# Kernel tuning notes

Measured on AMD Instinct MI355X. Metric: run time of the kernel, lower is better.

The kernel has to match this reference:

```python
import jax, jax.numpy as jnp
import numpy as np

C = 256; G = 8; K = 3; P = K * K; GC = C // G
PAD = K // 2; PAD_DW = 1
EPS_LN = 1e-5; EPS_DWLN = 1e-6; EPS_BN = 1e-5
OFFSET_SCALE = 1.0


def _ln(x, g, b, eps=EPS_LN):
    mu = x.mean(-1, keepdims=True)
    var = ((x - mu) ** 2).mean(-1, keepdims=True)
    return (x - mu) * jax.lax.rsqrt(var + eps) * g + b


def _bn(x, g, b, m, v):  # x: NCHW, eval-mode batchnorm with running stats
    s = jax.lax.rsqrt(v + EPS_BN)
    return (x - m[None, :, None, None]) * (g * s)[None, :, None, None] + b[None, :, None, None]


def _dcnv3_core(x, offset, mask):
    # x: (N,H,W,C) projected input; offset: (N,H,W,G*P*2); mask: (N,H,W,G,P) softmaxed
    N, H, W, _ = x.shape
    Hp, Wp = H + 2 * PAD, W + 2 * PAD
    x_pad = jnp.pad(x, ((0, 0), (PAD, PAD), (PAD, PAD), (0, 0)))
    img = x_pad.reshape(N, Hp, Wp, G, GC).transpose(0, 3, 4, 1, 2)  # (N,G,gc,Hp,Wp)
    # reference points, normalized by padded spatial dims (stride=1, dilation=1)
    start = (K - 1) // 2 + 0.5
    ref_x = (start + jnp.arange(W, dtype=x.dtype)) / Wp
    ref_y = (start + jnp.arange(H, dtype=x.dtype)) / Hp
    rx, ry = jnp.meshgrid(ref_x, ref_y, indexing='xy')  # (H,W)
    ref = jnp.stack([rx, ry], -1)  # (H,W,2) as (x,y)
    # dilation grid (kernel tap offsets), tap index p = i_w*K + j_h per torch meshgrid order
    gw = (jnp.arange(K, dtype=x.dtype) - (K - 1) // 2) / Wp
    gh = (jnp.arange(K, dtype=x.dtype) - (K - 1) // 2) / Hp
    gxx, gyy = jnp.meshgrid(gw, gh, indexing='ij')
    grid = jnp.stack([gxx, gyy], -1).reshape(P, 2)
    norm = jnp.array([Wp, Hp], dtype=x.dtype)
    off = offset.reshape(N, H, W, G, P, 2) * (OFFSET_SCALE / norm)
    loc = ref[None, :, :, None, None, :] + grid * OFFSET_SCALE + off  # (N,H,W,G,P,2)
    sg = (2.0 * loc - 1.0).transpose(0, 3, 1, 2, 4, 5).reshape(N, G, H * W, P, 2)

    def sample_one(im, gr):  # im: (gc,Hp,Wp), gr: (HW,P,2) in [-1,1]
        gx = (gr[..., 0] + 1.0) * (Wp / 2) - 0.5  # align_corners=False
        gy = (gr[..., 1] + 1.0) * (Hp / 2) - 0.5
        x0 = jnp.floor(gx); y0 = jnp.floor(gy)
        wx = gx - x0; wy = gy - y0
        def gat(ix, iy):
            valid = ((ix >= 0) & (ix <= Wp - 1) & (iy >= 0) & (iy <= Hp - 1)).astype(im.dtype)
            ixc = jnp.clip(ix, 0, Wp - 1).astype(jnp.int32)
            iyc = jnp.clip(iy, 0, Hp - 1).astype(jnp.int32)
            return im[:, iyc, ixc] * valid  # (gc,HW,P), zero padding outside
        return (gat(x0, y0) * ((1 - wx) * (1 - wy))
                + gat(x0 + 1, y0) * (wx * (1 - wy))
                + gat(x0, y0 + 1) * ((1 - wx) * wy)
                + gat(x0 + 1, y0 + 1) * (wx * wy))

    sampled = jax.vmap(jax.vmap(sample_one))(img, sg)  # (N,G,gc,HW,P)
    m = mask.transpose(0, 3, 1, 2, 4).reshape(N, G, 1, H * W, P)
    out = (sampled * m).sum(-1)  # (N,G,gc,HW)
    return out.transpose(0, 3, 1, 2).reshape(N, H, W, C)


def _dcnv3(inp, dw_w, dw_b, dwln_g, dwln_b, off_w, off_b, msk_w, msk_b, inp_w, inp_b, outp_w, outp_b):
    N, H, W, _ = inp.shape
    x = inp @ inp_w + inp_b  # input_proj
    # depthwise conv offset/mask branch (on the raw input, not the projection)
    x1 = jax.lax.conv_general_dilated(inp, dw_w, (1, 1), ((PAD_DW, PAD_DW), (PAD_DW, PAD_DW)),
                                      dimension_numbers=('NHWC', 'HWIO', 'NHWC'),
                                      feature_group_count=C) + dw_b
    x1 = jax.nn.gelu(_ln(x1, dwln_g, dwln_b, EPS_DWLN), approximate=False)
    offset = x1 @ off_w + off_b  # (N,H,W,G*P*2)
    mask = jax.nn.softmax((x1 @ msk_w + msk_b).reshape(N, H, W, G, P), axis=-1)
    return _dcnv3_core(x, offset, mask) @ outp_w + outp_b  # output_proj


def _forward(x, conv1_w, bn1_g, bn1_b, bn1_m, bn1_v, ln1_g, ln1_b, dw_w, dw_b, dwln_g, dwln_b,
             off_w, off_b, msk_w, msk_b, inp_w, inp_b, outp_w, outp_b, gamma1,
             ln2_g, ln2_b, fc1_w, fc1_b, fc2_w, fc2_b, gamma2, bn2_g, bn2_b, bn2_m, bn2_v):
    out = jax.lax.conv_general_dilated(x, conv1_w, (1, 1), ((1, 1), (1, 1)),
                                       dimension_numbers=('NCHW', 'OIHW', 'NCHW'))
    out = jax.nn.relu(_bn(out, bn1_g, bn1_b, bn1_m, bn1_v))
    t = out.transpose(0, 2, 3, 1)  # NHWC for the InternImage layer
    # post_norm InternImage layer with layer_scale
    d = _dcnv3(t, dw_w, dw_b, dwln_g, dwln_b, off_w, off_b, msk_w, msk_b, inp_w, inp_b, outp_w, outp_b)
    t = t + gamma1 * _ln(d, ln1_g, ln1_b)
    h = jax.nn.gelu(t @ fc1_w + fc1_b, approximate=False) @ fc2_w + fc2_b
    t = t + gamma2 * _ln(h, ln2_g, ln2_b)
    out = _bn(t.transpose(0, 3, 1, 2), bn2_g, bn2_b, bn2_m, bn2_v)
    return jax.nn.relu(out + x)  # residual (downsample is None: stride=1, inplanes==planes)


def setup_inputs() -> dict:
    key = jax.random.key(0)
    ks = iter(jax.random.split(key, 48))
    rn = lambda shape, s=1.0: jax.random.normal(next(ks), shape, dtype=jnp.float32) * s
    hid = 4 * C
    d = {}
    d['x'] = rn((8, C, 56, 56))
    d['conv1_w'] = rn((C, C, 3, 3), (2.0 / (9 * C)) ** 0.5)
    d['bn1_g'] = jnp.ones((C,), jnp.float32); d['bn1_b'] = jnp.zeros((C,), jnp.float32)
    d['bn1_m'] = rn((C,), 0.1)
    d['bn1_v'] = jax.random.uniform(next(ks), (C,), jnp.float32, 0.5, 1.5)
    d['ln1_g'] = jnp.ones((C,), jnp.float32); d['ln1_b'] = jnp.zeros((C,), jnp.float32)
    d['dw_w'] = rn((3, 3, 1, C), (1.0 / 9) ** 0.5); d['dw_b'] = jnp.zeros((C,), jnp.float32)
    d['dwln_g'] = jnp.ones((C,), jnp.float32); d['dwln_b'] = jnp.zeros((C,), jnp.float32)
    d['off_w'] = rn((C, G * P * 2), 0.01); d['off_b'] = rn((G * P * 2,), 0.01)
    d['msk_w'] = rn((C, G * P), 0.01); d['msk_b'] = jnp.zeros((G * P,), jnp.float32)
    d['inp_w'] = rn((C, C), C ** -0.5); d['inp_b'] = jnp.zeros((C,), jnp.float32)
    d['outp_w'] = rn((C, C), C ** -0.5); d['outp_b'] = jnp.zeros((C,), jnp.float32)
    d['gamma1'] = rn((C,), 0.01)
    d['ln2_g'] = jnp.ones((C,), jnp.float32); d['ln2_b'] = jnp.zeros((C,), jnp.float32)
    d['fc1_w'] = rn((C, hid), C ** -0.5); d['fc1_b'] = jnp.zeros((hid,), jnp.float32)
    d['fc2_w'] = rn((hid, C), hid ** -0.5); d['fc2_b'] = jnp.zeros((C,), jnp.float32)
    d['gamma2'] = rn((C,), 0.01)
    d['bn2_g'] = jnp.ones((C,), jnp.float32); d['bn2_b'] = jnp.zeros((C,), jnp.float32)
    d['bn2_m'] = rn((C,), 0.1)
    d['bn2_v'] = jax.random.uniform(next(ks), (C,), jnp.float32, 0.5, 1.5)
    return d


def reference(x, conv1_w, bn1_g, bn1_b, bn1_m, bn1_v, ln1_g, ln1_b, dw_w, dw_b, dwln_g, dwln_b,
              off_w, off_b, msk_w, msk_b, inp_w, inp_b, outp_w, outp_b, gamma1,
              ln2_g, ln2_b, fc1_w, fc1_b, fc2_w, fc2_b, gamma2, bn2_g, bn2_b, bn2_m, bn2_v):
    return _forward(x, conv1_w, bn1_g, bn1_b, bn1_m, bn1_v, ln1_g, ln1_b, dw_w, dw_b, dwln_g, dwln_b,
                    off_w, off_b, msk_w, msk_b, inp_w, inp_b, outp_w, outp_b, gamma1,
                    ln2_g, ln2_b, fc1_w, fc1_b, fc2_w, fc2_b, gamma2, bn2_g, bn2_b, bn2_m, bn2_v)
```

## Files before the change

### kernel.cpp

```cpp
#include <hip/hip_runtime.h>
#include <cmath>

#define N_   8
#define H_   56
#define W_   56
#define C_   256
#define HW_  3136
#define NHW_ 25088
#define G_   8
#define GC_  32
#define P_   9
#define HID_ 1024
#define XP_H 58
#define XP_W 58

typedef __attribute__((ext_vector_type(8))) short bf16x8;
typedef __attribute__((ext_vector_type(4))) float f32x4;

#define GLOAD_LDS16(g, l) __builtin_amdgcn_global_load_lds( \
    (const __attribute__((address_space(1))) void*)(g), \
    (__attribute__((address_space(3))) void*)(l), 16, 0, 0)

__device__ __forceinline__ unsigned short f2bf(float f) {
    unsigned u = __float_as_uint(f);
    u += 0x7FFF + ((u >> 16) & 1);
    return (unsigned short)(u >> 16);
}

__device__ __forceinline__ float gelu_exact(float v) {
    return 0.5f * v * (1.f + erff(v * 0.70710678118654752f));
}

__device__ __forceinline__ float2 block_sum2(float a, float b, float* sm) {
    int lane = threadIdx.x & 63;
    int wid  = threadIdx.x >> 6;
#pragma unroll
    for (int off = 32; off > 0; off >>= 1) {
        a += __shfl_down(a, off, 64);
        b += __shfl_down(b, off, 64);
    }
    if (lane == 0) { sm[wid] = a; sm[wid + 4] = b; }
    __syncthreads();
    float ra = sm[0] + sm[1] + sm[2] + sm[3];
    float rb = sm[4] + sm[5] + sm[6] + sm[7];
    __syncthreads();
    return make_float2(ra, rb);
}

__global__ __launch_bounds__(256) void k_prep_xpad(const float* __restrict__ x, unsigned short* __restrict__ xpad) {
    int nh = blockIdx.x;
    int n = nh / H_, h = nh - n * H_;
    int c = threadIdx.x;
    const float* xr = x + ((size_t)(n * C_ + c)) * HW_ + h * W_;
    unsigned short* orow = xpad + ((size_t)((n * XP_H + h + 1) * XP_W + 1)) * C_ + c;
    for (int w = 0; w < W_; ++w) orow[(size_t)w * C_] = f2bf(xr[w]);
}

__global__ __launch_bounds__(256) void k_prep_wTT(const float* __restrict__ w, unsigned short* __restrict__ wTT) {
    int i  = blockIdx.x * 256 + threadIdx.x;
    int ci = i & 255;
    int r  = i >> 8;
    int co = r & 255;
    int kk = r >> 8;
    wTT[i] = f2bf(w[(co * 256 + ci) * 9 + kk]);
}

__global__ __launch_bounds__(256) void k_prep_sqT(const float* __restrict__ src, unsigned short* __restrict__ dst) {
    int n = blockIdx.x, k = threadIdx.x;
    dst[n * C_ + k] = f2bf(src[k * C_ + n]);
}

__global__ __launch_bounds__(256) void k_prep_fc1T(const float* __restrict__ src, unsigned short* __restrict__ dst) {
    int n = blockIdx.x, k = threadIdx.x;
    dst[(size_t)n * C_ + k] = f2bf(src[(size_t)k * HID_ + n]);
}

__global__ __launch_bounds__(256) void k_prep_fc2T(const float* __restrict__ src, unsigned short* __restrict__ dst) {
    int n = blockIdx.x, k0 = threadIdx.x;
#pragma unroll
    for (int q = 0; q < 4; ++q) {
        int k = q * 256 + k0;
        dst[(size_t)n * HID_ + k] = f2bf(src[(size_t)k * C_ + n]);
    }
}

__global__ __launch_bounds__(256) void k_prep_om(const float* __restrict__ offw, const float* __restrict__ offb,
                                                 const float* __restrict__ mskw, const float* __restrict__ mskb,
                                                 unsigned short* __restrict__ omT, float* __restrict__ omb) {
    int n = blockIdx.x, k = threadIdx.x;
    float v = 0.f;
    if (n < 144)      v = offw[k * 144 + n];
    else if (n < 216) v = mskw[k * 72 + (n - 144)];
    omT[n * C_ + k] = f2bf(v);
    if (k == 0) omb[n] = (n < 144) ? offb[n] : (n < 216 ? mskb[n - 144] : 0.f);
}

__global__ __launch_bounds__(256) void k_conv1_mfma(const unsigned short* __restrict__ xpad,
                                                    const unsigned short* __restrict__ wTT,
                                                    const float* __restrict__ g, const float* __restrict__ b,
                                                    const float* __restrict__ m, const float* __restrict__ v,
                                                    float* __restrict__ t, unsigned short* __restrict__ t_bf) {
    __shared__ __align__(16) unsigned char smem[24576];
    unsigned short* sm16 = (unsigned short*)smem;
    bf16x8* sA = (bf16x8*)smem;
    bf16x8* sB = (bf16x8*)(smem + 8192);
    int tid = threadIdx.x;
    int wave = tid >> 6, lane = tid & 63;
    int r = lane & 15, kq = lane >> 4;
    int mt = blockIdx.x >> 1, nt = blockIdx.x & 1;
    int m0 = mt * 64, n0 = nt * 128;
    int wm = wave & 1, wn = wave >> 1;

    int pix = m0 + wave * 16 + r;
    int n = pix / HW_, hw = pix - n * HW_;
    int h = hw / W_, w = hw - h * W_;
    size_t abase = ((size_t)((n * XP_H + h) * XP_W + w)) * C_;

    f32x4 acc[2][4] = {};
#pragma unroll 1
    for (int kt = 0; kt < 36; ++kt) {
        int tap = kt >> 2, ktk = kt & 3;
        int kh = tap / 3, kw = tap - kh * 3;
        int k0 = ktk * 64;
        const unsigned short* ap = xpad + abase + (size_t)(kh * XP_W + kw) * C_ + k0;
        if (kt) __syncthreads();
#pragma unroll
        for (int i = 0; i < 2; ++i) {
            int q = wave * 2 + i;
            GLOAD_LDS16(ap + (i * 4 + kq) * 8, sm16 + q * 512);
        }
#pragma unroll
        for (int i = 0; i < 4; ++i) {
            int q = wave * 4 + i;
            int nrow = n0 + (q >> 1) * 16 + r;
            int cc   = (q & 1) * 4 + kq;
            GLOAD_LDS16(wTT + ((size_t)(tap * C_) + nrow) * C_ + k0 + cc * 8, sm16 + 4096 + q * 512);
        }
        __syncthreads();
#pragma unroll
        for (int ks = 0; ks < 2; ++ks) {
            bf16x8 af[2], bfr[4];
#pragma unroll
            for (int mi = 0; mi < 2; ++mi) af[mi]  = sA[((wm * 2 + mi) * 2 + ks) * 64 + lane];
#pragma unroll
            for (int ni = 0; ni < 4; ++ni) bfr[ni] = sB[((wn * 4 + ni) * 2 + ks) * 64 + lane];
#pragma unroll
            for (int mi = 0; mi < 2; ++mi)
#pragma unroll
                for (int ni = 0; ni < 4; ++ni)
                    acc[mi][ni] = __builtin_amdgcn_mfma_f32_16x16x32_bf16(af[mi], bfr[ni], acc[mi][ni], 0, 0, 0);
        }
    }

#pragma unroll
    for (int ni = 0; ni < 4; ++ni) {
        int co = n0 + (wn * 4 + ni) * 16 + r;
        float sc = g[co] * rsqrtf(v[co] + 1e-5f);
        float sh = b[co] - m[co] * sc;
#pragma unroll
        for (int mi = 0; mi < 2; ++mi) {
#pragma unroll
            for (int reg = 0; reg < 4; ++reg) {
                int po = m0 + (wm * 2 + mi) * 16 + kq * 4 + reg;
                float val = fmaxf(acc[mi][ni][reg] * sc + sh, 0.f);
                size_t idx = (size_t)po * C_ + co;
                t[idx] = val;
                t_bf[idx] = f2bf(val);
            }
        }
    }
}

__global__ __launch_bounds__(256) void k_inproj_mfma(const unsigned short* __restrict__ t_bf,
                                                     const unsigned short* __restrict__ inpwT,
                                                     const float* __restrict__ bias,
                                                     float* __restrict__ xproj) {
    int wave = threadIdx.x >> 6, lane = threadIdx.x & 63;
    int r = lane & 15, kq = lane >> 4;
    int p0 = blockIdx.x * 32, co0 = wave * 64;
    f32x4 acc[2][4] = {};
#pragma unroll 1
    for (int ks = 0; ks < 8; ++ks) {
        bf16x8 a0 = *(const bf16x8*)(t_bf + (size_t)(p0 + r) * C_ + ks * 32 + kq * 8);
        bf16x8 a1 = *(const bf16x8*)(t_bf + (size_t)(p0 + 16 + r) * C_ + ks * 32 + kq * 8);
        const unsigned short* bp = inpwT + (size_t)(co0 + r) * C_ + ks * 32 + kq * 8;
#pragma unroll
        for (int ni = 0; ni < 4; ++ni) {
            bf16x8 b = *(const bf16x8*)(bp + (size_t)ni * 16 * C_);
            acc[0][ni] = __builtin_amdgcn_mfma_f32_16x16x32_bf16(a0, b, acc[0][ni], 0, 0, 0);
            acc[1][ni] = __builtin_amdgcn_mfma_f32_16x16x32_bf16(a1, b, acc[1][ni], 0, 0, 0);
        }
    }
#pragma unroll
    for (int ni = 0; ni < 4; ++ni) {
        int col = co0 + ni * 16 + r;
        float bb = bias[col];
#pragma unroll
        for (int mi = 0; mi < 2; ++mi)
#pragma unroll
            for (int reg = 0; reg < 4; ++reg) {
                int pix = p0 + mi * 16 + kq * 4 + reg;
                xproj[(size_t)pix * C_ + col] = acc[mi][ni][reg] + bb;
            }
    }
}

__global__ __launch_bounds__(256) void k_dw(const float* __restrict__ t, const float* __restrict__ dww,
                                            const float* __restrict__ dwb, const float* __restrict__ lg,
                                            const float* __restrict__ lb, unsigned short* __restrict__ x1_bf) {
    __shared__ float sm[8];
    int pix = blockIdx.x;
    int n = pix / HW_, hw = pix - n * HW_;
    int h = hw / W_,  w = hw - h * W_;
    int c = threadIdx.x;
    float acc = dwb[c];
#pragma unroll
    for (int kh = 0; kh < 3; ++kh) {
        int y = h + kh - 1;
        if ((unsigned)y >= H_) continue;
#pragma unroll
        for (int kw = 0; kw < 3; ++kw) {
            int xx = w + kw - 1;
            if ((unsigned)xx >= W_) continue;
            acc = fmaf(t[(size_t)(n * HW_ + y * W_ + xx) * C_ + c], dww[(kh * 3 + kw) * C_ + c], acc);
        }
    }
    float2 r  = block_sum2(acc, acc * acc, sm);
    float mu  = r.x * (1.f / C_);
    float var = fmaxf(r.y * (1.f / C_) - mu * mu, 0.f);
    float rs  = rsqrtf(var + 1e-6f);
    float val = (acc - mu) * rs * lg[c] + lb[c];
    x1_bf[(size_t)pix * C_ + c] = f2bf(gelu_exact(val));
}

__global__ __launch_bounds__(256) void k_offmask_mfma(const unsigned short* __restrict__ x1_bf,
                                                      const unsigned short* __restrict__ omT,
                                                      const float* __restrict__ omb,
                                                      float* __restrict__ offo, float* __restrict__ msko) {
    __shared__ float som[32][225];
    int wave = threadIdx.x >> 6, lane = threadIdx.x & 63;
    int r = lane & 15, kq = lane >> 4;
    int p0 = blockIdx.x * 32, co0 = wave * 64;
    f32x4 acc[2][4] = {};
#pragma unroll 1
    for (int ks = 0; ks < 8; ++ks) {
        bf16x8 a0 = *(const bf16x8*)(x1_bf + (size_t)(p0 + r) * C_ + ks * 32 + kq * 8);
        bf16x8 a1 = *(const bf16x8*)(x1_bf + (size_t)(p0 + 16 + r) * C_ + ks * 32 + kq * 8);
        const unsigned short* bp = omT + (size_t)(co0 + r) * C_ + ks * 32 + kq * 8;
#pragma unroll
        for (int ni = 0; ni < 4; ++ni) {
            bf16x8 b = *(const bf16x8*)(bp + (size_t)ni * 16 * C_);
            acc[0][ni] = __builtin_amdgcn_mfma_f32_16x16x32_bf16(a0, b, acc[0][ni], 0, 0, 0);
            acc[1][ni] = __builtin_amdgcn_mfma_f32_16x16x32_bf16(a1, b, acc[1][ni], 0, 0, 0);
        }
    }
#pragma unroll
    for (int ni = 0; ni < 4; ++ni) {
        int col = co0 + ni * 16 + r;
        if (col < 216) {
            float bb = omb[col];
#pragma unroll
            for (int mi = 0; mi < 2; ++mi)
#pragma unroll
                for (int reg = 0; reg < 4; ++reg)
                    som[mi * 16 + kq * 4 + reg][col] = acc[mi][ni][reg] + bb;
        }
    }
    __syncthreads();
    int tid = threadIdx.x;
#pragma unroll
    for (int i = 0; i < 18; ++i) {
        int j = i * 256 + tid;
        int px = j / 144, col = j - px * 144;
        offo[(size_t)(p0 + px) * 144 + col] = som[px][col];
    }
    int px = tid >> 3, g = tid & 7;
    float mx = -1e30f;
#pragma unroll
    for (int p = 0; p < 9; ++p) mx = fmaxf(mx, som[px][144 + g * 9 + p]);
    float e[9], s = 0.f;
#pragma unroll
    for (int p = 0; p < 9; ++p) { e[p] = expf(som[px][144 + g * 9 + p] - mx); s += e[p]; }
    float inv = 1.f / s;
#pragma unroll
    for (int p = 0; p < 9; ++p) msko[(size_t)(p0 + px) * 72 + g * 9 + p] = e[p] * inv;
}

__global__ __launch_bounds__(256) void k_core(const float* __restrict__ xp,
                                              const float* __restrict__ offo, const float* __restrict__ msko,
                                              unsigned short* __restrict__ core_bf) {
    int pix = blockIdx.x;
    int n = pix / HW_, hw = pix - n * HW_;
    int h = hw / W_,  w = hw - h * W_;
    int g  = threadIdx.x >> 5;
    int cc = threadIdx.x & 31;
    const float* op = offo + (size_t)pix * 144 + g * 18;
    const float* mp = msko + (size_t)pix * 72 + g * 9;
    const float* xg = xp + (size_t)n * HW_ * C_ + g * GC_ + cc;
    float acc = 0.f;
#pragma unroll
    for (int p = 0; p < 9; ++p) {
        float gx = (float)(w + (p / 3)) + op[p * 2];
        float gy = (float)(h + (p % 3)) + op[p * 2 + 1];
        float fx = floorf(gx), fy = floorf(gy);
        float wx = gx - fx,   wy = gy - fy;
        int ix = (int)fx - 1, iy = (int)fy - 1;
        float v00 = 0.f, v10 = 0.f, v01 = 0.f, v11 = 0.f;
        bool x0ok = (unsigned)ix < W_, x1ok = (unsigned)(ix + 1) < W_;
        bool y0ok = (unsigned)iy < H_, y1ok = (unsigned)(iy + 1) < H_;
        if (y0ok) {
            const float* rr = xg + (size_t)(iy * W_) * C_;
            if (x0ok) v00 = rr[(size_t)ix * C_];
            if (x1ok) v10 = rr[(size_t)(ix + 1) * C_];
        }
        if (y1ok) {
            const float* rr = xg + (size_t)((iy + 1) * W_) * C_;
            if (x0ok) v01 = rr[(size_t)ix * C_];
            if (x1ok) v11 = rr[(size_t)(ix + 1) * C_];
        }
        float sval = (v00 * (1.f - wx) + v10 * wx) * (1.f - wy)
                   + (v01 * (1.f - wx) + v11 * wx) * wy;
        acc = fmaf(mp[p], sval, acc);
    }
    core_bf[(size_t)pix * C_ + threadIdx.x] = f2bf(acc);
}

__global__ __launch_bounds__(256) void k_outproj_mfma(const unsigned short* __restrict__ core_bf,
                                                      const unsigned short* __restrict__ outpwT,
                                                      const float* __restrict__ bo,
                                                      const float* __restrict__ g1, const float* __restrict__ lg,
                                                      const float* __restrict__ lb,
                                                      float* __restrict__ t, unsigned short* __restrict__ t_bf) {
    __shared__ float sd[32][260];
    int wave = threadIdx.x >> 6, lane = threadIdx.x & 63;
    int r = lane & 15, kq = lane >> 4;
    int p0 = blockIdx.x * 32, co0 = wave * 64;
    f32x4 acc[2][4] = {};
#pragma unroll 1
    for (int ks = 0; ks < 8; ++ks) {
        bf16x8 a0 = *(const bf16x8*)(core_bf + (size_t)(p0 + r) * C_ + ks * 32 + kq * 8);
        bf16x8 a1 = *(const bf16x8*)(core_bf + (size_t)(p0 + 16 + r) * C_ + ks * 32 + kq * 8);
        const unsigned short* bp = outpwT + (size_t)(co0 + r) * C_ + ks * 32 + kq * 8;
#pragma unroll
        for (int ni = 0; ni < 4; ++ni) {
            bf16x8 b = *(const bf16x8*)(bp + (size_t)ni * 16 * C_);
            acc[0][ni] = __builtin_amdgcn_mfma_f32_16x16x32_bf16(a0, b, acc[0][ni], 0, 0, 0);
            acc[1][ni] = __builtin_amdgcn_mfma_f32_16x16x32_bf16(a1, b, acc[1][ni], 0, 0, 0);
        }
    }
#pragma unroll
    for (int ni = 0; ni < 4; ++ni) {
        int col = co0 + ni * 16 + r;
        float bb = bo[col];
#pragma unroll
        for (int mi = 0; mi < 2; ++mi)
#pragma unroll
            for (int reg = 0; reg < 4; ++reg)
                sd[mi * 16 + kq * 4 + reg][col] = acc[mi][ni][reg] + bb;
    }
    __syncthreads();
    int px = threadIdx.x >> 3, sub = threadIdx.x & 7;
    float s1 = 0.f, s2 = 0.f;
#pragma unroll
    for (int i = 0; i < 8; ++i) {
        float4 vv = *(const float4*)&sd[px][sub * 32 + i * 4];
        s1 += vv.x + vv.y + vv.z + vv.w;
        s2 += vv.x * vv.x + vv.y * vv.y + vv.z * vv.z + vv.w * vv.w;
    }
#pragma unroll
    for (int off = 1; off < 8; off <<= 1) { s1 += __shfl_xor(s1, off, 64); s2 += __shfl_xor(s2, off, 64); }
    float mu  = s1 * (1.f / C_);
    float var = fmaxf(s2 * (1.f / C_) - mu * mu, 0.f);
    float rs  = rsqrtf(var + 1e-5f);
#pragma unroll
    for (int i = 0; i < 32; ++i) {
        int col = sub * 32 + i;
        size_t idx = (size_t)(p0 + px) * C_ + col;
        float tn = t[idx] + g1[col] * ((sd[px][col] - mu) * rs * lg[col] + lb[col]);
        t[idx] = tn;
        t_bf[idx] = f2bf(tn);
    }
}

__global__ __launch_bounds__(256) void k_fc1_mfma(const unsigned short* __restrict__ t_bf,
                                                  const unsigned short* __restrict__ fc1wT,
                                                  const float* __restrict__ fc1b,
                                                  unsigned short* __restrict__ h_bf) {
    __shared__ __align__(16) unsigned char smem[34816];
    unsigned short* sm16 = (unsigned short*)smem;
    bf16x8* sA = (bf16x8*)smem;
    bf16x8* sB = (bf16x8*)(smem + 16384);
    int tid = threadIdx.x;
    int wave = tid >> 6, lane = tid & 63;
    int r = lane & 15, kq = lane >> 4;
    int mt = blockIdx.x >> 3, nt = blockIdx.x & 7;
    int m0 = mt * 128, n0 = nt * 128;
    int wm = wave & 1, wn = wave >> 1;

    f32x4 acc[4][4] = {};
#pragma unroll 1
    for (int kt = 0; kt < 4; ++kt) {
        int k0 = kt * 64;
        if (kt) __syncthreads();
#pragma unroll
        for (int i = 0; i < 4; ++i) {
            int q = wave * 4 + i;
            int row = m0 + (q >> 1) * 16 + r;
            int cc  = (q & 1) * 4 + kq;
            GLOAD_LDS16(t_bf + (size_t)row * C_ + k0 + cc * 8, sm16 + q * 512);
        }
#pragma unroll
        for (int i = 0; i < 4; ++i) {
            int q = wave * 4 + i;
            int nrow = n0 + (q >> 1) * 16 + r;
            int cc   = (q & 1) * 4 + kq;
            GLOAD_LDS16(fc1wT + (size_t)nrow * C_ + k0 + cc * 8, sm16 + 8192 + q * 512);
        }
        __syncthreads();
#pragma unroll
        for (int ks = 0; ks < 2; ++ks) {
            bf16x8 af[4], bfr[4];
#pragma unroll
            for (int mi = 0; mi < 4; ++mi) af[mi]  = sA[((wm * 4 + mi) * 2 + ks) * 64 + lane];
#pragma unroll
            for (int ni = 0; ni < 4; ++ni) bfr[ni] = sB[((wn * 4 + ni) * 2 + ks) * 64 + lane];
#pragma unroll
            for (int mi = 0; mi < 4; ++mi)
#pragma unroll
                for (int ni = 0; ni < 4; ++ni)
                    acc[mi][ni] = __builtin_amdgcn_mfma_f32_16x16x32_bf16(af[mi], bfr[ni], acc[mi][ni], 0, 0, 0);
        }
    }
    __syncthreads();
#pragma unroll
    for (int ni = 0; ni < 4; ++ni) {
        int col = (wn * 4 + ni) * 16 + r;
        float bb = fc1b[n0 + col];
#pragma unroll
        for (int mi = 0; mi < 4; ++mi)
#pragma unroll
            for (int reg = 0; reg < 4; ++reg) {
                int row = (wm * 4 + mi) * 16 + kq * 4 + reg;
                sm16[row * 136 + col] = f2bf(gelu_exact(acc[mi][ni][reg] + bb));
            }
    }
    __syncthreads();
    int trow = tid >> 1, thalf = tid & 1;
    const unsigned short* src = sm16 + trow * 136 + thalf * 64;
    unsigned short* dst = h_bf + (size_t)(m0 + trow) * HID_ + n0 + thalf * 64;
#pragma unroll
    for (int j = 0; j < 8; ++j)
        *(bf16x8*)(dst + j * 8) = *(const bf16x8*)(src + j * 8);
}

__global__ __launch_bounds__(256) void k_fc2ln_mfma(const unsigned short* __restrict__ h_bf,
                                                    const unsigned short* __restrict__ fc2wT,
                                                    const float* __restrict__ fc2b,
                                                    const float* __restrict__ g2, const float* __restrict__ lg,
                                                    const float* __restrict__ lb, float* __restrict__ t) {
    __shared__ __align__(16) unsigned char smem[40960];
    unsigned short* sm16 = (unsigned short*)smem;
    bf16x8* sA = (bf16x8*)smem;
    bf16x8* sB = (bf16x8*)(smem + 8192);
    int tid = threadIdx.x;
    int wave = tid >> 6, lane = tid & 63;
    int r = lane & 15, kq = lane >> 4;
    int m0 = blockIdx.x * 64;

    f32x4 acc[16] = {};
#pragma unroll 1
    for (int kt = 0; kt < 16; ++kt) {
        int k0 = kt * 64;
        if (kt) __syncthreads();
#pragma unroll
        for (int i = 0; i < 2; ++i) {
            int q = wave * 2 + i;
            int row = m0 + (q >> 1) * 16 + r;
            int cc  = (q & 1) * 4 + kq;
            GLOAD_LDS16(h_bf + (size_t)row * HID_ + k0 + cc * 8, sm16 + q * 512);
        }
#pragma unroll
        for (int i = 0; i < 8; ++i) {
            int q = wave * 8 + i;
            int nrow = (q >> 1) * 16 + r;
            int cc   = (q & 1) * 4 + kq;
            GLOAD_LDS16(fc2wT + (size_t)nrow * HID_ + k0 + cc * 8, sm16 + 4096 + q * 512);
        }
        __syncthreads();
#pragma unroll
        for (int ks = 0; ks < 2; ++ks) {
            bf16x8 a = sA[(wave * 2 + ks) * 64 + lane];
#pragma unroll
            for (int ni = 0; ni < 16; ++ni) {
                bf16x8 b = sB[(ni * 2 + ks) * 64 + lane];
                acc[ni] = __builtin_amdgcn_mfma_f32_16x16x32_bf16(a, b, acc[ni], 0, 0, 0);
            }
        }
    }
    float bb[16], g2v[16], lgv[16], lbv[16];
#pragma unroll
    for (int ni = 0; ni < 16; ++ni) {
        int col = ni * 16 + r;
        bb[ni] = fc2b[col]; g2v[ni] = g2[col]; lgv[ni] = lg[col]; lbv[ni] = lb[col];
    }
#pragma unroll
    for (int ni = 0; ni < 16; ++ni)
#pragma unroll
        for (int reg = 0; reg < 4; ++reg) acc[ni][reg] += bb[ni];
#pragma unroll
    for (int reg = 0; reg < 4; ++reg) {
        float s1 = 0.f, s2 = 0.f;
#pragma unroll
        for (int ni = 0; ni < 16; ++ni) { float vv = acc[ni][reg]; s1 += vv; s2 += vv * vv; }
#pragma unroll
        for (int off = 1; off < 16; off <<= 1) { s1 += __shfl_xor(s1, off, 64); s2 += __shfl_xor(s2, off, 64); }
        float mu  = s1 * (1.f / C_);
        float var = fmaxf(s2 * (1.f / C_) - mu * mu, 0.f);
        float rs  = rsqrtf(var + 1e-5f);
        int row = m0 + wave * 16 + kq * 4 + reg;
        float* tr = t + (size_t)row * C_;
#pragma unroll
        for (int ni = 0; ni < 16; ++ni) {
            int col = ni * 16 + r;
            tr[col] += g2v[ni] * ((acc[ni][reg] - mu) * rs * lgv[ni] + lbv[ni]);
        }
    }
}

__global__ __launch_bounds__(256) void k_final(const float* __restrict__ t, const float* __restrict__ x,
                                               const float* __restrict__ g, const float* __restrict__ b,
                                               const float* __restrict__ m, const float* __restrict__ v,
                                               float* __restrict__ out) {
    int i  = blockIdx.x * 256 + threadIdx.x;
    int hw = i % HW_;
    int r  = i / HW_;
    int c  = r & 255;
    int n  = r >> 8;
    float tv  = t[(size_t)(n * HW_ + hw) * C_ + c];
    float s   = rsqrtf(v[c] + 1e-5f);
    float val = (tv - m[c]) * (g[c] * s) + b[c] + x[i];
    out[i] = fmaxf(val, 0.f);
}

extern "C" void kernel_launch(void* const* d_in, const int* in_sizes, int n_in,
                              void* d_out, int out_size, void* d_ws, size_t ws_size,
                              hipStream_t stream) {
    const float* x      = (const float*)d_in[0];
    const float* conv1w = (const float*)d_in[1];
    const float* bn1g   = (const float*)d_in[2];
    const float* bn1b   = (const float*)d_in[3];
    const float* bn1m   = (const float*)d_in[4];
    const float* bn1v   = (const float*)d_in[5];
    const float* ln1g   = (const float*)d_in[6];
    const float* ln1b   = (const float*)d_in[7];
    const float* dww    = (const float*)d_in[8];
    const float* dwb    = (const float*)d_in[9];
    const float* dwlng  = (const float*)d_in[10];
    const float* dwlnb  = (const float*)d_in[11];
    const float* offw   = (const float*)d_in[12];
    const float* offb   = (const float*)d_in[13];
    const float* mskw   = (const float*)d_in[14];
    const float* mskb   = (const float*)d_in[15];
    const float* inpw   = (const float*)d_in[16];
    const float* inpb   = (const float*)d_in[17];
    const float* outpw  = (const float*)d_in[18];
    const float* outpb  = (const float*)d_in[19];
    const float* gamma1 = (const float*)d_in[20];
    const float* ln2g   = (const float*)d_in[21];
    const float* ln2b   = (const float*)d_in[22];
    const float* fc1w   = (const float*)d_in[23];
    const float* fc1b   = (const float*)d_in[24];
    const float* fc2w   = (const float*)d_in[25];
    const float* fc2b   = (const float*)d_in[26];
    const float* gamma2 = (const float*)d_in[27];
    const float* bn2g   = (const float*)d_in[28];
    const float* bn2b   = (const float*)d_in[29];
    const float* bn2m   = (const float*)d_in[30];
    const float* bn2v   = (const float*)d_in[31];
    float* out = (float*)d_out;

    float* ws    = (float*)d_ws;
    float* xproj = ws;
    float* offo  = xproj + (size_t)NHW_ * C_;
    float* msko  = offo  + (size_t)NHW_ * 144;
    unsigned short* x1_bf = (unsigned short*)(msko + (size_t)NHW_ * 72);
    unsigned short* scr   = x1_bf + (size_t)NHW_ * C_;
    float* t     = (float*)(scr + (size_t)N_ * XP_H * XP_W * C_);
    float* omb   = t + (size_t)NHW_ * C_;
    unsigned short* t_bf  = (unsigned short*)(omb + 256);
    unsigned short* wTT   = t_bf  + (size_t)NHW_ * C_;
    unsigned short* inpwT = wTT   + (size_t)9 * C_ * C_;
    unsigned short* outpwT= inpwT + (size_t)C_ * C_;
    unsigned short* fc1wT = outpwT+ (size_t)C_ * C_;
    unsigned short* fc2wT = fc1wT + (size_t)HID_ * C_;
    unsigned short* omT   = fc2wT + (size_t)C_ * HID_;
    unsigned short* xpad    = scr;
    unsigned short* core_bf = scr;
    unsigned short* h_bf    = (unsigned short*)xproj;

    hipMemsetAsync(xpad, 0, (size_t)N_ * XP_H * XP_W * C_ * sizeof(unsigned short), stream);
    k_prep_xpad<<<N_ * H_, 256, 0, stream>>>(x, xpad);
    k_prep_wTT <<<2304,    256, 0, stream>>>(conv1w, wTT);
    k_prep_sqT <<<256,     256, 0, stream>>>(inpw, inpwT);
    k_prep_sqT <<<256,     256, 0, stream>>>(outpw, outpwT);
    k_prep_fc1T<<<1024,    256, 0, stream>>>(fc1w, fc1wT);
    k_prep_fc2T<<<256,     256, 0, stream>>>(fc2w, fc2wT);
    k_prep_om  <<<256,     256, 0, stream>>>(offw, offb, mskw, mskb, omT, omb);

    k_conv1_mfma  <<<(NHW_ / 64) * 2, 256, 0, stream>>>(xpad, wTT, bn1g, bn1b, bn1m, bn1v, t, t_bf);
    k_inproj_mfma <<<NHW_ / 32, 256, 0, stream>>>(t_bf, inpwT, inpb, xproj);
    k_dw          <<<NHW_,      256, 0, stream>>>(t, dww, dwb, dwlng, dwlnb, x1_bf);
    k_offmask_mfma<<<NHW_ / 32, 256, 0, stream>>>(x1_bf, omT, omb, offo, msko);
    k_core        <<<NHW_,      256, 0, stream>>>(xproj, offo, msko, core_bf);
    k_outproj_mfma<<<NHW_ / 32, 256, 0, stream>>>(core_bf, outpwT, outpb, gamma1, ln1g, ln1b, t, t_bf);
    k_fc1_mfma    <<<(NHW_ / 128) * 8, 256, 0, stream>>>(t_bf, fc1wT, fc1b, h_bf);
    k_fc2ln_mfma  <<<NHW_ / 64, 256, 0, stream>>>(h_bf, fc2wT, fc2b, gamma2, ln2g, ln2b, t);
    k_final       <<<NHW_,      256, 0, stream>>>(t, x, bn2g, bn2b, bn2m, bn2v, out);
}
```

Measured before the change: 657.8 us.

## Double-buffer LDS staging in conv1 and fc2 GEMMs; restructure inproj to LDS

Conv1 and fc2+LN GEMMs now prefetch the next K-tile into a second LDS buffer using async global-to-LDS loads with explicit vmcnt waits, so loads overlap with MFMA work. The in-projection kernel is rewritten from direct global fragment loads into a 64-row-tile, LDS-staged, double-buffered GEMM like fc2. This hides global load latency at the cost of larger LDS allocations, up to 80KB per block, which may reduce occupancy. The inproj grid shrinks to 64-pixel tiles.

Measured after the change: 647.0 us. About the same (-1.6%).

```diff
diff --git a/kernel.cpp b/kernel.cpp
--- a/kernel.cpp
+++ b/kernel.cpp
@@ -100,10 +100,8 @@
                                                     const float* __restrict__ g, const float* __restrict__ b,
                                                     const float* __restrict__ m, const float* __restrict__ v,
                                                     float* __restrict__ t, unsigned short* __restrict__ t_bf) {
-    __shared__ __align__(16) unsigned char smem[24576];
+    __shared__ __align__(16) unsigned char smem[49152];
     unsigned short* sm16 = (unsigned short*)smem;
-    bf16x8* sA = (bf16x8*)smem;
-    bf16x8* sB = (bf16x8*)(smem + 8192);
     int tid = threadIdx.x;
     int wave = tid >> 6, lane = tid & 63;
     int r = lane & 15, kq = lane >> 4;
@@ -117,26 +115,39 @@
     size_t abase = ((size_t)((n * XP_H + h) * XP_W + w)) * C_;
 
     f32x4 acc[2][4] = {};
-#pragma unroll 1
-    for (int kt = 0; kt < 36; ++kt) {
+
+    auto stage = [&](int kt, int buf) {
         int tap = kt >> 2, ktk = kt & 3;
         int kh = tap / 3, kw = tap - kh * 3;
         int k0 = ktk * 64;
+        unsigned short* dstA = sm16 + buf * 12288;
+        unsigned short* dstB = dstA + 4096;
         const unsigned short* ap = xpad + abase + (size_t)(kh * XP_W + kw) * C_ + k0;
-        if (kt) __syncthreads();
-#pragma unroll
-        for (int i = 0; i < 2; ++i) {
-            int q = wave * 2 + i;
-            GLOAD_LDS16(ap + (i * 4 + kq) * 8, sm16 + q * 512);
-        }
+#pragma unroll
+        for (int i = 0; i < 2; ++i)
+            GLOAD_LDS16(ap + (i * 4 + kq) * 8, dstA + (wave * 2 + i) * 512);
 #pragma unroll
         for (int i = 0; i < 4; ++i) {
             int q = wave * 4 + i;
             int nrow = n0 + (q >> 1) * 16 + r;
             int cc   = (q & 1) * 4 + kq;
-            GLOAD_LDS16(wTT + ((size_t)(tap * C_) + nrow) * C_ + k0 + cc * 8, sm16 + 4096 + q * 512);
-        }
-        __syncthreads();
+            GLOAD_LDS16(wTT + ((size_t)(tap * C_) + nrow) * C_ + k0 + cc * 8, dstB + q * 512);
+        }
+    };
+
+    stage(0, 0);
+    int cur = 0;
+#pragma unroll 1
+    for (int kt = 0; kt < 36; ++kt) {
+        if (kt < 35) {
+            stage(kt + 1, cur ^ 1);
+            asm volatile("s_waitcnt vmcnt(6)" ::: "memory");
+        } else {
+            asm volatile("s_waitcnt vmcnt(0)" ::: "memory");
+        }
+        __builtin_amdgcn_s_barrier();
+        bf16x8* sA = (bf16x8*)(sm16 + cur * 12288);
+        bf16x8* sB = sA + 512;
 #pragma unroll
         for (int ks = 0; ks < 2; ++ks) {
             bf16x8 af[2], bfr[4];
@@ -150,6 +161,8 @@
                 for (int ni = 0; ni < 4; ++ni)
                     acc[mi][ni] = __builtin_amdgcn_mfma_f32_16x16x32_bf16(af[mi], bfr[ni], acc[mi][ni], 0, 0, 0);
         }
+        __builtin_amdgcn_s_barrier();
+        cur ^= 1;
     }
 
 #pragma unroll
@@ -175,33 +188,69 @@
                                                      const unsigned short* __restrict__ inpwT,
                                                      const float* __restrict__ bias,
                                                      float* __restrict__ xproj) {
-    int wave = threadIdx.x >> 6, lane = threadIdx.x & 63;
+    __shared__ __align__(16) unsigned char smem[81920];
+    unsigned short* sm16 = (unsigned short*)smem;
+    int tid = threadIdx.x;
+    int wave = tid >> 6, lane = tid & 63;
     int r = lane & 15, kq = lane >> 4;
-    int p0 = blockIdx.x * 32, co0 = wave * 64;
-    f32x4 acc[2][4] = {};
+    int m0 = blockIdx.x * 64;
+
+    f32x4 acc[16] = {};
+
+    auto stage = [&](int kt, int buf) {
+        int k0 = kt * 64;
+        unsigned short* dstA = sm16 + buf * 20480;
+        unsigned short* dstB = dstA + 4096;
+#pragma unroll
+        for (int i = 0; i < 2; ++i) {
+            int q = wave * 2 + i;
+            int row = m0 + wave * 16 + r;
+            GLOAD_LDS16(t_bf + (size_t)row * C_ + k0 + (i * 4 + kq) * 8, dstA + q * 512);
+        }
+#pragma unroll
+        for (int i = 0; i < 8; ++i) {
+            int q = wave * 8 + i;
+            int nrow = (q >> 1) * 16 + r;
+            int cc   = (q & 1) * 4 + kq;
+            GLOAD_LDS16(inpwT + (size_t)nrow * C_ + k0 + cc * 8, dstB + q * 512);
+        }
+    };
+
+    stage(0, 0);
+    int cur = 0;
 #pragma unroll 1
-    for (int ks = 0; ks < 8; ++ks) {
-        bf16x8 a0 = *(const bf16x8*)(t_bf + (size_t)(p0 + r) * C_ + ks * 32 + kq * 8);
-        bf16x8 a1 = *(const bf16x8*)(t_bf + (size_t)(p0 + 16 + r) * C_ + ks * 32 + kq * 8);
-        const unsigned short* bp = inpwT + (size_t)(co0 + r) * C_ + ks * 32 + kq * 8;
-#pragma unroll
-        for (int ni = 0; ni < 4; ++ni) {
-            bf16x8 b = *(const bf16x8*)(bp + (size_t)ni * 16 * C_);
-            acc[0][ni] = __builtin_amdgcn_mfma_f32_16x16x32_bf16(a0, b, acc[0][ni], 0, 0, 0);
-            acc[1][ni] = __builtin_amdgcn_mfma_f32_16x16x32_bf16(a1, b, acc[1][ni], 0, 0, 0);
-        }
-    }
-#pragma unroll
-    for (int ni = 0; ni < 4; ++ni) {
-        int col = co0 + ni * 16 + r;
+    for (int kt = 0; kt < 4; ++kt) {
+        if (kt < 3) {
+            stage(kt + 1, cur ^ 1);
+            asm volatile("s_waitcnt vmcnt(10)" ::: "memory");
+        } else {
+            asm volatile("s_waitcnt vmcnt(0)" ::: "memory");
+        }
+        __builtin_amdgcn_s_barrier();
+        bf16x8* sA = (bf16x8*)(sm16 + cur * 20480);
+        bf16x8* sB = sA + 512;
+#pragma unroll
+        for (int ks = 0; ks < 2; ++ks) {
+            bf16x8 a = sA[(wave * 2 + ks) * 64 + lane];
+#pragma unroll
+            for (int ni = 0; ni < 16; ++ni) {
+                bf16x8 b = sB[(ni * 2 + ks) * 64 + lane];
+                acc[ni] = __builtin_amdgcn_mfma_f32_16x16x32_bf16(a, b, acc[ni], 0, 0, 0);
+            }
+        }
+        __builtin_amdgcn_s_barrier();
+        cur ^= 1;
+    }
+
+#pragma unroll
+    for (int ni = 0; ni < 16; ++ni) {
+        int col = ni * 16 + r;
         float bb = bias[col];
 #pragma unroll
-        for (int mi = 0; mi < 2; ++mi)
-#pragma unroll
-            for (int reg = 0; reg < 4; ++reg) {
-                int pix = p0 + mi * 16 + kq * 4 + reg;
-                xproj[(size_t)pix * C_ + col] = acc[mi][ni][reg] + bb;
-            }
+        for (int reg = 0; reg < 4; ++reg) {
+            int row = m0 + wave * 16 + kq * 4 + reg;
+            xproj[(size_t)row * C_ + col] = acc[ni][reg] + bb;
+        }
     }
 }
 
@@ -458,35 +507,47 @@
                                                     const float* __restrict__ fc2b,
                                                     const float* __restrict__ g2, const float* __restrict__ lg,
                                                     const float* __restrict__ lb, float* __restrict__ t) {
-    __shared__ __align__(16) unsigned char smem[40960];
+    __shared__ __align__(16) unsigned char smem[81920];
     unsigned short* sm16 = (unsigned short*)smem;
-    bf16x8* sA = (bf16x8*)smem;
-    bf16x8* sB = (bf16x8*)(smem + 8192);
     int tid = threadIdx.x;
     int wave = tid >> 6, lane = tid & 63;
     int r = lane & 15, kq = lane >> 4;
     int m0 = blockIdx.x * 64;
 
     f32x4 acc[16] = {};
-#pragma unroll 1
-    for (int kt = 0; kt < 16; ++kt) {
+
+    auto stage = [&](int kt, int buf) {
         int k0 = kt * 64;
-        if (kt) __syncthreads();
+        unsigned short* dstA = sm16 + buf * 20480;
+        unsigned short* dstB = dstA + 4096;
 #pragma unroll
         for (int i = 0; i < 2; ++i) {
             int q = wave * 2 + i;
-            int row = m0 + (q >> 1) * 16 + r;
-            int cc  = (q & 1) * 4 + kq;
-            GLOAD_LDS16(h_bf + (size_t)row * HID_ + k0 + cc * 8, sm16 + q * 512);
+            int row = m0 + wave * 16 + r;
+            GLOAD_LDS16(h_bf + (size_t)row * HID_ + k0 + (i * 4 + kq) * 8, dstA + q * 512);
         }
 #pragma unroll
         for (int i = 0; i < 8; ++i) {
             int q = wave * 8 + i;
             int nrow = (q >> 1) * 16 + r;
             int cc   = (q & 1) * 4 + kq;
-            GLOAD_LDS16(fc2wT + (size_t)nrow * HID_ + k0 + cc * 8, sm16 + 4096 + q * 512);
-        }
-        __syncthreads();
+            GLOAD_LDS16(fc2wT + (size_t)nrow * HID_ + k0 + cc * 8, dstB + q * 512);
+        }
+    };
+
+    stage(0, 0);
+    int cur = 0;
+#pragma unroll 1
+    for (int kt = 0; kt < 16; ++kt) {
+        if (kt < 15) {
+            stage(kt + 1, cur ^ 1);
+            asm volatile("s_waitcnt vmcnt(10)" ::: "memory");
+        } else {
+            asm volatile("s_waitcnt vmcnt(0)" ::: "memory");
+        }
+        __builtin_amdgcn_s_barrier();
+        bf16x8* sA = (bf16x8*)(sm16 + cur * 20480);
+        bf16x8* sB = sA + 512;
 #pragma unroll
         for (int ks = 0; ks < 2; ++ks) {
             bf16x8 a = sA[(wave * 2 + ks) * 64 + lane];
@@ -496,6 +557,8 @@
                 acc[ni] = __builtin_amdgcn_mfma_f32_16x16x32_bf16(a, b, acc[ni], 0, 0, 0);
             }
         }
+        __builtin_amdgcn_s_barrier();
+        cur ^= 1;
     }
     float bb[16], g2v[16], lgv[16], lbv[16];
 #pragma unroll
@@ -608,7 +671,7 @@
     k_prep_om  <<<256,     256, 0, stream>>>(offw, offb, mskw, mskb, omT, omb);
 
     k_conv1_mfma  <<<(NHW_ / 64) * 2, 256, 0, stream>>>(xpad, wTT, bn1g, bn1b, bn1m, bn1v, t, t_bf);
-    k_inproj_mfma <<<NHW_ / 32, 256, 0, stream>>>(t_bf, inpwT, inpb, xproj);
+    k_inproj_mfma <<<NHW_ / 64, 256, 0, stream>>>(t_bf, inpwT, inpb, xproj);
     k_dw          <<<NHW_,      256, 0, stream>>>(t, dww, dwb, dwlng, dwlnb, x1_bf);
     k_offmask_mfma<<<NHW_ / 32, 256, 0, stream>>>(x1_bf, omT, omb, offo, msko);
     k_core        <<<NHW_,      256, 0, stream>>>(xproj, offo, msko, core_bf);
```
